# Performance work log

Measured on AMD Instinct MI355X. Metric: run time of the kernel, lower is better.

## Reference

```python
import jax, jax.numpy as jnp
import numpy as np

N = 2048       # x_dim (input features)
M = 2048       # y_dim (output features)
R0 = 1024      # components in table 0 (knn table)
D_K = 1024     # key encoder embed dim
D_V = 1024     # val encoder embed dim
BATCH = 512
ISTA_ALPHA = 1.0
ISTA_MAXITER = 5


def _ortho_encoder(key, n, d):
    # get_embedding_matrix with ortho=True: QR of (s,s) gaussian, take [:n,:d]
    s = max(n, d)
    q = jnp.linalg.qr(jax.random.normal(key, (s, s), dtype=jnp.float32))[0]
    return q[:n, :d]


def setup_inputs() -> dict:
    key = jax.random.key(0)
    kw, kk, kv, kx = jax.random.split(key, 4)
    W = jax.random.normal(kw, (N, M), dtype=jnp.float32) / np.float32(np.sqrt(N))
    # torch: V, S, U = svd(W); U = U.T  -> V = left vecs (n,k), U = right vecs (m,k)
    Usvd, S, Vh = jnp.linalg.svd(W, full_matrices=False)
    V = Usvd          # (n, k)
    Ur = Vh.T         # (m, k)
    key_enc = _ortho_encoder(kk, N, D_K)   # (n, d_k)
    val_enc = _ortho_encoder(kv, M, D_V)   # (m, d_v)
    # table 0: knn table over components [0:R0]
    keys_t0 = V[:, :R0].T @ key_enc        # (R0, d_k)
    vals_t0 = Ur[:, :R0].T @ val_enc       # (R0, d_v)
    scales_t0 = S[:R0][:, None]            # (R0, 1)
    # table 1: plain low-rank table over components [R0:]
    keys_t1 = V[:, R0:]                    # (n, R1)
    vals_t1 = Ur[:, R0:]                   # (m, R1)
    scales_t1 = S[R0:][:, None]            # (R1, 1)
    x = jax.random.normal(kx, (BATCH, N), dtype=jnp.float32)
    return {"x": x, "key_enc": key_enc, "val_enc": val_enc,
            "keys_t0": keys_t0, "vals_t0": vals_t0, "scales_t0": scales_t0,
            "keys_t1": keys_t1, "vals_t1": vals_t1, "scales_t1": scales_t1}


def _soft(x, t):
    return jnp.sign(x) * jnp.maximum(jnp.abs(x) - t, 0.0)


def reference(x, key_enc, val_enc, keys_t0, vals_t0, scales_t0,
              keys_t1, vals_t1, scales_t1):
    # --- table 0: knn path (batched; original looped over batch samples) ---
    q = x @ key_enc                        # (B, d_k)
    alphas = q @ keys_t0.T                 # (B, R0)
    betas = alphas * scales_t0.T           # (B, R0)
    yb = betas @ vals_t0                   # (B, d_v)
    # ISTA: min ||yb - z @ val_enc||^2 + alpha*||z||_1, step=1 (val_enc has
    # orthonormal columns so Lipschitz const of grad is 1)
    z = yb @ val_enc.T                     # z0, (B, m)
    for _ in range(ISTA_MAXITER):
        z = _soft(z + (yb - z @ val_enc) @ val_enc.T, ISTA_ALPHA)
    y = z                                  # knn path assigns y[b,:] = yh
    # --- table 1: low-rank path (accumulates) ---
    alphas2 = x @ keys_t1                  # (B, R1)
    betas2 = alphas2 * scales_t1.T         # (B, R1)
    y = y + betas2 @ vals_t1.T             # (B, m)
    return y
```

## Files before the change

### kernel.cpp

```cpp
#include <hip/hip_runtime.h>


typedef _Float16 f16x8 __attribute__((ext_vector_type(8)));
typedef _Float16 f16x4 __attribute__((ext_vector_type(4)));
typedef float f32x4 __attribute__((ext_vector_type(4)));

enum { EPI_H, EPI_QOFF, EPI_SPLIT, EPI_SOFT, EPI_YP, EPI_ZQ, EPI_ZQFO };

typedef const __attribute__((address_space(1))) void* gas_ptr;
typedef __attribute__((address_space(3))) void* las_ptr;

__device__ __forceinline__ void gload16(const void* g, void* l) {
  __builtin_amdgcn_global_load_lds((gas_ptr)g, (las_ptr)l, 16, 0, 0);
}

__device__ __forceinline__ float softt(float t) {
  float s = fabsf(t) - 1.0f;
  s = s > 0.0f ? s : 0.0f;
  return copysignf(s, t);
}

__global__ __launch_bounds__(256) void convAll(
    const float* __restrict__ e0, const float* __restrict__ e1,
    const float* __restrict__ e2, const float* __restrict__ e3,
    _Float16* __restrict__ o0, _Float16* __restrict__ o1,
    _Float16* __restrict__ o2, _Float16* __restrict__ o3,
    const float* __restrict__ s1, const float* __restrict__ s2,
    const float4* __restrict__ pa, f16x4* __restrict__ qa, int na,
    const float4* __restrict__ pb, f16x4* __restrict__ qb, int nb,
    const float4* __restrict__ pc, f16x4* __restrict__ qc, int nc) {
  const int z = blockIdx.z;
  if (z == 4) {
    const int total = na + nb + nc;
    const int bid = blockIdx.y * 32 + blockIdx.x;
    const int nthr = 2048 * 256;
    for (int i = bid * 256 + threadIdx.y * 32 + threadIdx.x; i < total;
         i += nthr) {
      const float4* s;
      f16x4* d;
      int j = i;
      if (j < na) {
        s = pa; d = qa;
      } else if ((j -= na) < nb) {
        s = pb; d = qb;
      } else {
        j -= nb; s = pc; d = qc;
      }
      float4 v = s[j];
      f16x4 h = {(_Float16)v.x, (_Float16)v.y, (_Float16)v.z, (_Float16)v.w};
      d[j] = h;
    }
    return;
  }
  const float* in = z == 0 ? e0 : z == 1 ? e1 : z == 2 ? e2 : e3;
  _Float16* out = z == 0 ? o0 : z == 1 ? o1 : z == 2 ? o2 : o3;
  const int R = (z < 2) ? 2048 : 1024;
  const int C = 1024;
  const int mode = z == 1 ? 1 : z == 2 ? 2 : 0;
  const float* sv = z == 1 ? s1 : s2;
  __shared__ float t[32][33];
  const int tx = threadIdx.x, ty = threadIdx.y;
  const int c0 = blockIdx.x * 32, r0 = blockIdx.y * 32;
  if (r0 >= R) return;
#pragma unroll
  for (int i = 0; i < 32; i += 8)
    t[ty + i][tx] = in[(size_t)(r0 + ty + i) * C + c0 + tx];
  __syncthreads();
#pragma unroll
  for (int i = 0; i < 32; i += 8) {
    float v = t[tx][ty + i];
    if (mode == 1) v *= sv[c0 + ty + i];
    if (mode == 2) v *= sv[r0 + tx];
    out[(size_t)(c0 + ty + i) * R + r0 + tx] = (_Float16)v;
  }
}

template <int EPI>
__device__ __forceinline__ void gtile(
    const _Float16* __restrict__ A, int lda, const _Float16* __restrict__ B,
    int ldb, int nK, int N, int brow, int bcol, float* __restrict__ dgout,
    _Float16* __restrict__ oh, _Float16* __restrict__ oh2, _Float16* sm,
    int tid) {
  const int lane = tid & 63;
  const int w = tid >> 6;
  const int wr = w & 1;
  const int wk = w >> 1;
  const int srow = lane >> 3;
  const int scol = ((lane & 7) ^ srow) << 3;
  const int a15 = lane & 15;
  const int hi = lane >> 4;
  const int l7 = lane & 7;

  const _Float16* apg = A + (size_t)(brow + (w << 4) + srow) * lda + scol;
  const _Float16* bpg = B + (size_t)(bcol + (w << 4) + srow) * ldb + scol;
  _Float16* AB = sm;
  _Float16* BB = sm + 16384;
  const int ldstA = w << 10;

  const int ca = ((wk << 2) + hi) ^ l7;
  int raddr[2], baddr[4];
#pragma unroll
  for (int mi = 0; mi < 2; ++mi)
    raddr[mi] = ((wr << 5) + (mi << 4) + a15) * 64 + (ca << 3);
#pragma unroll
  for (int ni = 0; ni < 4; ++ni)
    baddr[ni] = ((ni << 4) + a15) * 64 + (ca << 3);

  f32x4 acc[2][4] = {};

  __syncthreads();

#pragma unroll
  for (int p = 0; p < 2; ++p) {
    gload16(apg + p * 64, AB + p * 4096 + ldstA);
    gload16(apg + p * 64 + (size_t)8 * lda, AB + p * 4096 + ldstA + 512);
    gload16(bpg + p * 64, BB + p * 4096 + ldstA);
    gload16(bpg + p * 64 + (size_t)8 * ldb, BB + p * 4096 + ldstA + 512);
  }

  for (int kt = 0; kt < nK; ++kt) {
    if (kt + 2 < nK) {
      const int bf = (kt + 2) & 3;
      const int co = (kt + 2) << 6;
      gload16(apg + co, AB + bf * 4096 + ldstA);
      gload16(apg + co + (size_t)8 * lda, AB + bf * 4096 + ldstA + 512);
      gload16(bpg + co, BB + bf * 4096 + ldstA);
      gload16(bpg + co + (size_t)8 * ldb, BB + bf * 4096 + ldstA + 512);
    }
    const int rem = nK - 1 - kt;
    if (rem >= 2)
      asm volatile("s_waitcnt vmcnt(8)" ::: "memory");
    else if (rem == 1)
      asm volatile("s_waitcnt vmcnt(4)" ::: "memory");
    else
      asm volatile("s_waitcnt vmcnt(0)" ::: "memory");
    __builtin_amdgcn_s_barrier();
    __builtin_amdgcn_sched_barrier(0);
    const _Float16* Ab = AB + (kt & 3) * 4096;
    const _Float16* Bb = BB + (kt & 3) * 4096;
    f16x8 av[2], bv[4];
    av[0] = *(const f16x8*)(Ab + raddr[0]);
    av[1] = *(const f16x8*)(Ab + raddr[1]);
    bv[0] = *(const f16x8*)(Bb + baddr[0]);
    bv[1] = *(const f16x8*)(Bb + baddr[1]);
    bv[2] = *(const f16x8*)(Bb + baddr[2]);
    bv[3] = *(const f16x8*)(Bb + baddr[3]);
#pragma unroll
    for (int mi = 0; mi < 2; ++mi)
#pragma unroll
      for (int ni = 0; ni < 4; ++ni)
        acc[mi][ni] = __builtin_amdgcn_mfma_f32_16x16x32_f16(
            av[mi], bv[ni], acc[mi][ni], 0, 0, 0);
  }

  __syncthreads();
  float* scr = (float*)sm;
  const int sl = (wr << 6) + lane;
  if (wk == 1) {
#pragma unroll
    for (int mi = 0; mi < 2; ++mi)
#pragma unroll
      for (int ni = 0; ni < 4; ++ni)
#pragma unroll
        for (int r = 0; r < 4; ++r)
          scr[(((mi << 2) + ni) * 4 + r) * 128 + sl] = acc[mi][ni][r];
  }
  __syncthreads();
  if (wk == 0) {
#pragma unroll
    for (int mi = 0; mi < 2; ++mi) {
#pragma unroll
      for (int ni = 0; ni < 4; ++ni) {
#pragma unroll
        for (int r = 0; r < 4; ++r) {
          const float v =
              acc[mi][ni][r] + scr[(((mi << 2) + ni) * 4 + r) * 128 + sl];
          const int row = brow + (wr << 5) + (mi << 4) + (hi << 2) + r;
          const int col = bcol + (ni << 4) + a15;
          const size_t idx = (size_t)row * N + col;
          if constexpr (EPI == EPI_H) {
            oh[idx] = (_Float16)v;
          } else if constexpr (EPI == EPI_QOFF) {
            if (row == col) {
              dgout[row] = 1.0f - v;
              oh[idx] = (_Float16)0.0f;
            } else {
              oh[idx] = (_Float16)(-v);
            }
          } else {
            if (col < 1024)
              oh[(size_t)row * 1024 + col] = (_Float16)v;
            else
              oh2[(size_t)row * 1024 + (col - 1024)] = (_Float16)v;
          }
        }
      }
    }
  }
}

template <int EPI>
__device__ __forceinline__ void gt32(
    const _Float16* __restrict__ A, int lda, const _Float16* __restrict__ B,
    int ldb, int nK, int N, int brow, int bcol, const float* __restrict__ dgv,
    float* __restrict__ fA, float* __restrict__ fB,
    _Float16* __restrict__ oh, const float* __restrict__ fC,
    float* __restrict__ ofin, _Float16* sm, int tid) {
  const int lane = tid & 63;
  const int w = tid >> 6;
  const int wc = w & 1;
  const int wk = w >> 1;
  const int srow = lane >> 3;
  const int scol = ((lane & 7) ^ srow) << 3;
  const int a15 = lane & 15, hi = lane >> 4, l7 = lane & 7;

  const _Float16* apg = A + (size_t)(brow + (w << 3) + srow) * lda + scol;
  const _Float16* bpg = B + (size_t)(bcol + (w << 4) + srow) * ldb + scol;
  _Float16* AB = sm;
  _Float16* BB = sm + 8192;
  const int ca = ((wk << 2) + hi) ^ l7;
  int raddr[2], baddr[2];
#pragma unroll
  for (int mi = 0; mi < 2; ++mi)
    raddr[mi] = ((mi << 4) + a15) * 64 + (ca << 3);
#pragma unroll
  for (int ni = 0; ni < 2; ++ni)
    baddr[ni] = ((wc << 5) + (ni << 4) + a15) * 64 + (ca << 3);

  f32x4 acc[2][2] = {};
  __syncthreads();

#pragma unroll
  for (int p = 0; p < 2; ++p) {
    gload16(apg + p * 64, AB + p * 2048 + (w << 9));
    gload16(bpg + p * 64, BB + p * 4096 + (w << 10));
    gload16(bpg + p * 64 + (size_t)8 * ldb, BB + p * 4096 + (w << 10) + 512);
  }
  for (int kt = 0; kt < nK; ++kt) {
    if (kt + 2 < nK) {
      const int bf = (kt + 2) & 3;
      const int co = (kt + 2) << 6;
      gload16(apg + co, AB + bf * 2048 + (w << 9));
      gload16(bpg + co, BB + bf * 4096 + (w << 10));
      gload16(bpg + co + (size_t)8 * ldb, BB + bf * 4096 + (w << 10) + 512);
    }
    const int rem = nK - 1 - kt;
    if (rem >= 2)
      asm volatile("s_waitcnt vmcnt(6)" ::: "memory");
    else if (rem == 1)
      asm volatile("s_waitcnt vmcnt(3)" ::: "memory");
    else
      asm volatile("s_waitcnt vmcnt(0)" ::: "memory");
    __builtin_amdgcn_s_barrier();
    __builtin_amdgcn_sched_barrier(0);
    const _Float16* Ab = AB + (kt & 3) * 2048;
    const _Float16* Bb = BB + (kt & 3) * 4096;
    f16x8 av[2], bv[2];
    av[0] = *(const f16x8*)(Ab + raddr[0]);
    av[1] = *(const f16x8*)(Ab + raddr[1]);
    bv[0] = *(const f16x8*)(Bb + baddr[0]);
    bv[1] = *(const f16x8*)(Bb + baddr[1]);
#pragma unroll
    for (int mi = 0; mi < 2; ++mi)
#pragma unroll
      for (int ni = 0; ni < 2; ++ni)
        acc[mi][ni] = __builtin_amdgcn_mfma_f32_16x16x32_f16(
            av[mi], bv[ni], acc[mi][ni], 0, 0, 0);
  }
  __syncthreads();
  float* scr = (float*)sm;
  const int sl = (wc << 6) + lane;
  if (wk == 1) {
#pragma unroll
    for (int mi = 0; mi < 2; ++mi)
#pragma unroll
      for (int ni = 0; ni < 2; ++ni)
#pragma unroll
        for (int r = 0; r < 4; ++r)
          scr[(((mi << 1) + ni) * 4 + r) * 128 + sl] = acc[mi][ni][r];
  }
  __syncthreads();
  if (wk == 0) {
#pragma unroll
    for (int mi = 0; mi < 2; ++mi) {
#pragma unroll
      for (int ni = 0; ni < 2; ++ni) {
#pragma unroll
        for (int r = 0; r < 4; ++r) {
          const float v =
              acc[mi][ni][r] + scr[(((mi << 1) + ni) * 4 + r) * 128 + sl];
          const int row = brow + (mi << 4) + (hi << 2) + r;
          const int col = bcol + (wc << 5) + (ni << 4) + a15;
          const size_t idx = (size_t)row * N + col;
          if constexpr (EPI == EPI_SOFT) {
            fA[idx] = v;
            float s = softt(v);
            fB[idx] = s;
            oh[idx] = (_Float16)s;
          } else if constexpr (EPI == EPI_YP) {
            ofin[idx] = v;
          } else if constexpr (EPI == EPI_ZQ) {
            float t = fA[idx] + dgv[col] * fB[idx] + v;
            float s = softt(t);
            fB[idx] = s;
            oh[idx] = (_Float16)s;
          } else {
            float t = fA[idx] + dgv[col] * fB[idx] + v;
            ofin[idx] = fC[idx] + softt(t);
          }
        }
      }
    }
  }
}

struct WS {
  const _Float16 *ve, *vt1, *w0pT_r, *Bcat, *qoff_r, *x, *kt0s, *vt0T, *w0_r,
      *q_r, *be2;
  _Float16 *w0pT_w, *qoff_w, *w0_w, *q_w, *be2_w, *zhA, *zhB;
  float *z0, *zf, *dg, *yp;
};

__device__ __forceinline__ void map512(int b, int& br, int& bc) {
  const int x = b & 7, i = b >> 3;
  bc = (x << 2) | (i & 3);
  br = i >> 2;
}

__global__ __launch_bounds__(256, 2) void kD2(WS p) {
  __shared__ __align__(16) _Float16 sm[32768];
  const int tid = threadIdx.x;
  const int bid = blockIdx.x;
  if (bid < 1024) {
    gtile<EPI_QOFF>(p.ve, 1024, p.ve, 1024, 16, 2048, (bid >> 5) << 6,
                    (bid & 31) << 6, p.dg, p.qoff_w, nullptr, sm, tid);
  } else if (bid < 1280) {
    const int i = bid - 1024;
    gtile<EPI_SPLIT>(p.x, 2048, p.Bcat, 2048, 32, 2048, (i >> 5) << 6,
                     (i & 31) << 6, nullptr, p.q_w, p.be2_w, sm, tid);
  } else {
    const int i = bid - 1280;
    gtile<EPI_H>(p.kt0s, 1024, p.vt0T, 1024, 16, 1024, (i >> 4) << 6,
                 (i & 15) << 6, nullptr, p.w0_w, nullptr, sm, tid);
  }
}

__global__ __launch_bounds__(256, 2) void kW0p(WS p) {
  __shared__ __align__(16) _Float16 sm[32768];
  const int x = blockIdx.x & 7, i = blockIdx.x >> 3;
  const int bc = (x << 1) | (i & 1), br = i >> 1;
  gtile<EPI_H>(p.ve, 1024, p.w0_r, 1024, 16, 1024, br << 6, bc << 6, nullptr,
               p.w0pT_w, nullptr, sm, threadIdx.x);
}

__global__ __launch_bounds__(256, 3) void kD4(WS p) {
  __shared__ __align__(16) _Float16 sm[24576];
  const int bid = blockIdx.x;
  int br, bc;
  if (bid < 512) {
    map512(bid, br, bc);
    gt32<EPI_SOFT>(p.q_r, 1024, p.w0pT_r, 1024, 16, 2048, br << 5, bc << 6,
                   nullptr, p.z0, p.zf, p.zhA, nullptr, nullptr, sm,
                   threadIdx.x);
  } else {
    map512(bid - 512, br, bc);
    gt32<EPI_YP>(p.be2, 1024, p.vt1, 1024, 16, 2048, br << 5, bc << 6,
                 nullptr, nullptr, nullptr, nullptr, nullptr, p.yp, sm,
                 threadIdx.x);
  }
}

template <bool AB>
__global__ __launch_bounds__(256, 2) void kZQ(WS p) {
  __shared__ __align__(16) _Float16 sm[24576];
  int br, bc;
  map512(blockIdx.x, br, bc);
  gt32<EPI_ZQ>(AB ? p.zhA : p.zhB, 2048, p.qoff_r, 2048, 32, 2048, br << 5,
               bc << 6, p.dg, p.z0, p.zf, AB ? p.zhB : p.zhA, nullptr,
               nullptr, sm, threadIdx.x);
}

__global__ __launch_bounds__(256, 2) void kZQF(WS p, float* out) {
  __shared__ __align__(16) _Float16 sm[24576];
  int br, bc;
  map512(blockIdx.x, br, bc);
  gt32<EPI_ZQFO>(p.zhB, 2048, p.qoff_r, 2048, 32, 2048, br << 5, bc << 6,
                 p.dg, p.z0, p.zf, nullptr, p.yp, out, sm, threadIdx.x);
}

extern "C" void kernel_launch(void* const* d_in, const int* in_sizes, int n_in,
                              void* d_out, int out_size, void* d_ws,
                              size_t ws_size, hipStream_t stream) {
  const float* x = (const float*)d_in[0];
  const float* key_enc = (const float*)d_in[1];
  const float* val_enc = (const float*)d_in[2];
  const float* keys_t0 = (const float*)d_in[3];
  const float* vals_t0 = (const float*)d_in[4];
  const float* scales_t0 = (const float*)d_in[5];
  const float* keys_t1 = (const float*)d_in[6];
  const float* vals_t1 = (const float*)d_in[7];
  const float* scales_t1 = (const float*)d_in[8];

  constexpr size_t M1 = 1048576;
  _Float16* ws = (_Float16*)d_ws;
  _Float16* ve_h = ws;
  float* yp = (float*)ws;
  _Float16* vt1_h = ws + 2 * M1;
  _Float16* w0pT = ws + 4 * M1;
  _Float16* Bcat = ws + 6 * M1;
  _Float16* zhA = ws + 6 * M1;
  float* z0_f = (float*)(ws + 7 * M1);
  _Float16* zhB = ws + 9 * M1;
  _Float16* qoff = ws + 10 * M1;
  _Float16* x_h = ws + 14 * M1;
  _Float16* kt0s = ws + 15 * M1;
  float* z_f = (float*)(ws + 15 * M1);
  _Float16* vt0T = ws + 16 * M1;
  _Float16* w0 = ws + 17 * M1;
  _Float16* q_h = ws + 18 * M1;
  _Float16* be2 = ws + 18 * M1 + 524288;
  float* dg = (float*)(ws + 19 * M1);

  WS p;
  p.ve = ve_h; p.vt1 = vt1_h; p.w0pT_r = w0pT; p.w0pT_w = w0pT;
  p.Bcat = Bcat; p.qoff_r = qoff; p.qoff_w = qoff; p.x = x_h;
  p.kt0s = kt0s; p.vt0T = vt0T; p.w0_r = w0; p.w0_w = w0;
  p.q_r = q_h; p.q_w = q_h; p.be2 = be2; p.be2_w = be2;
  p.zhA = zhA; p.zhB = zhB; p.z0 = z0_f; p.zf = z_f; p.dg = dg; p.yp = yp;

  convAll<<<dim3(32, 64, 5), dim3(32, 8), 0, stream>>>(
      key_enc, keys_t1, keys_t0, vals_t0, Bcat, Bcat + 2 * M1, kt0s, vt0T,
      scales_t1, scales_t0, (const float4*)x, (f16x4*)x_h, 262144,
      (const float4*)val_enc, (f16x4*)ve_h, 524288, (const float4*)vals_t1,
      (f16x4*)vt1_h, 524288);
  kD2<<<1536, 256, 0, stream>>>(p);
  kW0p<<<512, 256, 0, stream>>>(p);
  kD4<<<1024, 256, 0, stream>>>(p);
  kZQ<true><<<512, 256, 0, stream>>>(p);
  kZQ<false><<<512, 256, 0, stream>>>(p);
  kZQ<true><<<512, 256, 0, stream>>>(p);
  kZQF<<<512, 256, 0, stream>>>(p, (float*)d_out);
}
```

Baseline: 110.3 us.

## Rebalance QOFF Gram tiles across kD2/kD3/kD4 to even out launch loads

The 1024 QOFF tiles (val_enc Gram-based operator) move out of kD2. Half of them join the w0p GEMM in a new kD3 kernel, and the other half join kD4 next to the soft-threshold and low-rank GEMMs. This spreads work more evenly across the dependent launches and fills idle CUs in the smaller kernels. yp is moved to its own workspace region so it no longer aliases ve_h, which QOFF tiles in kD4 still read. kD4 now uses the larger shared buffer with occupancy 2, down from 3, which may lower occupancy for the gt32 tiles.

```diff
diff --git a/kernel.cpp b/kernel.cpp
--- a/kernel.cpp
+++ b/kernel.cpp
@@ -331,42 +331,50 @@
   __shared__ __align__(16) _Float16 sm[32768];
   const int tid = threadIdx.x;
   const int bid = blockIdx.x;
-  if (bid < 1024) {
-    gtile<EPI_QOFF>(p.ve, 1024, p.ve, 1024, 16, 2048, (bid >> 5) << 6,
-                    (bid & 31) << 6, p.dg, p.qoff_w, nullptr, sm, tid);
-  } else if (bid < 1280) {
-    const int i = bid - 1024;
-    gtile<EPI_SPLIT>(p.x, 2048, p.Bcat, 2048, 32, 2048, (i >> 5) << 6,
-                     (i & 31) << 6, nullptr, p.q_w, p.be2_w, sm, tid);
+  if (bid < 256) {
+    gtile<EPI_SPLIT>(p.x, 2048, p.Bcat, 2048, 32, 2048, (bid >> 5) << 6,
+                     (bid & 31) << 6, nullptr, p.q_w, p.be2_w, sm, tid);
   } else {
-    const int i = bid - 1280;
+    const int i = bid - 256;
     gtile<EPI_H>(p.kt0s, 1024, p.vt0T, 1024, 16, 1024, (i >> 4) << 6,
                  (i & 15) << 6, nullptr, p.w0_w, nullptr, sm, tid);
   }
 }
 
-__global__ __launch_bounds__(256, 2) void kW0p(WS p) {
+__global__ __launch_bounds__(256, 2) void kD3(WS p) {
   __shared__ __align__(16) _Float16 sm[32768];
-  const int x = blockIdx.x & 7, i = blockIdx.x >> 3;
-  const int bc = (x << 1) | (i & 1), br = i >> 1;
-  gtile<EPI_H>(p.ve, 1024, p.w0_r, 1024, 16, 1024, br << 6, bc << 6, nullptr,
-               p.w0pT_w, nullptr, sm, threadIdx.x);
-}
-
-__global__ __launch_bounds__(256, 3) void kD4(WS p) {
-  __shared__ __align__(16) _Float16 sm[24576];
+  const int tid = threadIdx.x;
+  const int bid = blockIdx.x;
+  if (bid < 512) {
+    const int x = bid & 7, i = bid >> 3;
+    const int bc = (x << 1) | (i & 1), br = i >> 1;
+    gtile<EPI_H>(p.ve, 1024, p.w0_r, 1024, 16, 1024, br << 6, bc << 6,
+                 nullptr, p.w0pT_w, nullptr, sm, tid);
+  } else {
+    const int i = bid - 512;
+    gtile<EPI_QOFF>(p.ve, 1024, p.ve, 1024, 16, 2048, (i >> 5) << 6,
+                    (i & 31) << 6, p.dg, p.qoff_w, nullptr, sm, tid);
+  }
+}
+
+__global__ __launch_bounds__(256, 2) void kD4(WS p) {
+  __shared__ __align__(16) _Float16 sm[32768];
+  const int tid = threadIdx.x;
   const int bid = blockIdx.x;
   int br, bc;
   if (bid < 512) {
     map512(bid, br, bc);
     gt32<EPI_SOFT>(p.q_r, 1024, p.w0pT_r, 1024, 16, 2048, br << 5, bc << 6,
-                   nullptr, p.z0, p.zf, p.zhA, nullptr, nullptr, sm,
-                   threadIdx.x);
+                   nullptr, p.z0, p.zf, p.zhA, nullptr, nullptr, sm, tid);
+  } else if (bid < 1024) {
+    const int i = bid - 512;
+    gtile<EPI_QOFF>(p.ve, 1024, p.ve, 1024, 16, 2048,
+                    (16 + (i >> 5)) << 6, (i & 31) << 6, p.dg, p.qoff_w,
+                    nullptr, sm, tid);
   } else {
-    map512(bid - 512, br, bc);
+    map512(bid - 1024, br, bc);
     gt32<EPI_YP>(p.be2, 1024, p.vt1, 1024, 16, 2048, br << 5, bc << 6,
-                 nullptr, nullptr, nullptr, nullptr, nullptr, p.yp, sm,
-                 threadIdx.x);
+                 nullptr, nullptr, nullptr, nullptr, nullptr, p.yp, sm, tid);
   }
 }
 
@@ -404,7 +412,6 @@
   constexpr size_t M1 = 1048576;
   _Float16* ws = (_Float16*)d_ws;
   _Float16* ve_h = ws;
-  float* yp = (float*)ws;
   _Float16* vt1_h = ws + 2 * M1;
   _Float16* w0pT = ws + 4 * M1;
   _Float16* Bcat = ws + 6 * M1;
@@ -420,6 +427,7 @@
   _Float16* q_h = ws + 18 * M1;
   _Float16* be2 = ws + 18 * M1 + 524288;
   float* dg = (float*)(ws + 19 * M1);
+  float* yp = (float*)(ws + 20 * M1);
 
   WS p;
   p.ve = ve_h; p.vt1 = vt1_h; p.w0pT_r = w0pT; p.w0pT_w = w0pT;
@@ -433,9 +441,9 @@
       scales_t1, scales_t0, (const float4*)x, (f16x4*)x_h, 262144,
       (const float4*)val_enc, (f16x4*)ve_h, 524288, (const float4*)vals_t1,
       (f16x4*)vt1_h, 524288);
-  kD2<<<1536, 256, 0, stream>>>(p);
-  kW0p<<<512, 256, 0, stream>>>(p);
-  kD4<<<1024, 256, 0, stream>>>(p);
+  kD2<<<512, 256, 0, stream>>>(p);
+  kD3<<<1024, 256, 0, stream>>>(p);
+  kD4<<<1536, 256, 0, stream>>>(p);
   kZQ<true><<<512, 256, 0, stream>>>(p);
   kZQ<false><<<512, 256, 0, stream>>>(p);
   kZQ<true><<<512, 256, 0, stream>>>(p);
```

Result: no change. 111.2 us (+0.9%).

## Switch GEMM tiles to 32x32x16 MFMA with four-way split-K reduction

Applied to the files above, without the earlier changes.

Both GEMM tile routines replace 16x16x32 MFMA with 32x32x16 MFMA. Each of the four waves now handles a distinct 16-element K slice of the 64-wide K tile, instead of two waves splitting M/N and two splitting K. The epilogue becomes a four-way reduction through shared memory, with two waves each finalizing half the outputs. This aims for larger MFMA shapes and fewer LDS fragment reads, at the cost of a heavier cross-wave reduction and more accumulator registers. It also lowers kD4 launch bounds from 3 to 2 blocks per CU.

```diff
diff --git a/kernel.cpp b/kernel.cpp
--- a/kernel.cpp
+++ b/kernel.cpp
@@ -4,6 +4,7 @@
 typedef _Float16 f16x8 __attribute__((ext_vector_type(8)));
 typedef _Float16 f16x4 __attribute__((ext_vector_type(4)));
 typedef float f32x4 __attribute__((ext_vector_type(4)));
+typedef float f32x16 __attribute__((ext_vector_type(16)));
 
 enum { EPI_H, EPI_QOFF, EPI_SPLIT, EPI_SOFT, EPI_YP, EPI_ZQ, EPI_ZQFO };
 
@@ -76,56 +77,55 @@
 }
 
 template <int EPI>
-__device__ __forceinline__ void gtile(
+__device__ __forceinline__ void g64(
     const _Float16* __restrict__ A, int lda, const _Float16* __restrict__ B,
     int ldb, int nK, int N, int brow, int bcol, float* __restrict__ dgout,
     _Float16* __restrict__ oh, _Float16* __restrict__ oh2, _Float16* sm,
     int tid) {
   const int lane = tid & 63;
   const int w = tid >> 6;
-  const int wr = w & 1;
-  const int wk = w >> 1;
   const int srow = lane >> 3;
   const int scol = ((lane & 7) ^ srow) << 3;
-  const int a15 = lane & 15;
-  const int hi = lane >> 4;
+  const int r31 = lane & 31;
+  const int hi5 = lane >> 5;
   const int l7 = lane & 7;
 
   const _Float16* apg = A + (size_t)(brow + (w << 4) + srow) * lda + scol;
   const _Float16* bpg = B + (size_t)(bcol + (w << 4) + srow) * ldb + scol;
   _Float16* AB = sm;
   _Float16* BB = sm + 16384;
-  const int ldstA = w << 10;
-
-  const int ca = ((wk << 2) + hi) ^ l7;
-  int raddr[2], baddr[4];
+  const int ldst = w << 10;
+
+  const int swz = ((w << 1) + hi5) ^ l7;
+  int raddr[2], baddr[2];
 #pragma unroll
   for (int mi = 0; mi < 2; ++mi)
-    raddr[mi] = ((wr << 5) + (mi << 4) + a15) * 64 + (ca << 3);
-#pragma unroll
-  for (int ni = 0; ni < 4; ++ni)
-    baddr[ni] = ((ni << 4) + a15) * 64 + (ca << 3);
-
-  f32x4 acc[2][4] = {};
+    raddr[mi] = ((mi << 5) + r31) * 64 + (swz << 3);
+#pragma unroll
+  for (int ni = 0; ni < 2; ++ni)
+    baddr[ni] = ((ni << 5) + r31) * 64 + (swz << 3);
+
+  f32x16 acc[2][2] = {};
 
   __syncthreads();
 
 #pragma unroll
   for (int p = 0; p < 2; ++p) {
-    gload16(apg + p * 64, AB + p * 4096 + ldstA);
-    gload16(apg + p * 64 + (size_t)8 * lda, AB + p * 4096 + ldstA + 512);
-    gload16(bpg + p * 64, BB + p * 4096 + ldstA);
-    gload16(bpg + p * 64 + (size_t)8 * ldb, BB + p * 4096 + ldstA + 512);
+    const int co = p << 6;
+    gload16(apg + co, AB + p * 4096 + ldst);
+    gload16(apg + co + (size_t)8 * lda, AB + p * 4096 + ldst + 512);
+    gload16(bpg + co, BB + p * 4096 + ldst);
+    gload16(bpg + co + (size_t)8 * ldb, BB + p * 4096 + ldst + 512);
   }
 
   for (int kt = 0; kt < nK; ++kt) {
     if (kt + 2 < nK) {
       const int bf = (kt + 2) & 3;
       const int co = (kt + 2) << 6;
-      gload16(apg + co, AB + bf * 4096 + ldstA);
-      gload16(apg + co + (size_t)8 * lda, AB + bf * 4096 + ldstA + 512);
-      gload16(bpg + co, BB + bf * 4096 + ldstA);
-      gload16(bpg + co + (size_t)8 * ldb, BB + bf * 4096 + ldstA + 512);
+      gload16(apg + co, AB + bf * 4096 + ldst);
+      gload16(apg + co + (size_t)8 * lda, AB + bf * 4096 + ldst + 512);
+      gload16(bpg + co, BB + bf * 4096 + ldst);
+      gload16(bpg + co + (size_t)8 * ldb, BB + bf * 4096 + ldst + 512);
     }
     const int rem = nK - 1 - kt;
     if (rem >= 2)
@@ -138,69 +138,88 @@
     __builtin_amdgcn_sched_barrier(0);
     const _Float16* Ab = AB + (kt & 3) * 4096;
     const _Float16* Bb = BB + (kt & 3) * 4096;
-    f16x8 av[2], bv[4];
+    f16x8 av[2], bv[2];
     av[0] = *(const f16x8*)(Ab + raddr[0]);
     av[1] = *(const f16x8*)(Ab + raddr[1]);
     bv[0] = *(const f16x8*)(Bb + baddr[0]);
     bv[1] = *(const f16x8*)(Bb + baddr[1]);
-    bv[2] = *(const f16x8*)(Bb + baddr[2]);
-    bv[3] = *(const f16x8*)(Bb + baddr[3]);
 #pragma unroll
     for (int mi = 0; mi < 2; ++mi)
 #pragma unroll
-      for (int ni = 0; ni < 4; ++ni)
-        acc[mi][ni] = __builtin_amdgcn_mfma_f32_16x16x32_f16(
+      for (int ni = 0; ni < 2; ++ni)
+        acc[mi][ni] = __builtin_amdgcn_mfma_f32_32x32x16_f16(
             av[mi], bv[ni], acc[mi][ni], 0, 0, 0);
   }
 
   __syncthreads();
   float* scr = (float*)sm;
-  const int sl = (wr << 6) + lane;
-  if (wk == 1) {
+  if (w >= 2) {
 #pragma unroll
     for (int mi = 0; mi < 2; ++mi)
 #pragma unroll
-      for (int ni = 0; ni < 4; ++ni)
-#pragma unroll
-        for (int r = 0; r < 4; ++r)
-          scr[(((mi << 2) + ni) * 4 + r) * 128 + sl] = acc[mi][ni][r];
-  }
-  __syncthreads();
-  if (wk == 0) {
-#pragma unroll
-    for (int mi = 0; mi < 2; ++mi) {
-#pragma unroll
-      for (int ni = 0; ni < 4; ++ni) {
-#pragma unroll
-        for (int r = 0; r < 4; ++r) {
-          const float v =
-              acc[mi][ni][r] + scr[(((mi << 2) + ni) * 4 + r) * 128 + sl];
-          const int row = brow + (wr << 5) + (mi << 4) + (hi << 2) + r;
-          const int col = bcol + (ni << 4) + a15;
-          const size_t idx = (size_t)row * N + col;
-          if constexpr (EPI == EPI_H) {
-            oh[idx] = (_Float16)v;
-          } else if constexpr (EPI == EPI_QOFF) {
-            if (row == col) {
-              dgout[row] = 1.0f - v;
-              oh[idx] = (_Float16)0.0f;
-            } else {
-              oh[idx] = (_Float16)(-v);
-            }
-          } else {
-            if (col < 1024)
-              oh[(size_t)row * 1024 + col] = (_Float16)v;
-            else
-              oh2[(size_t)row * 1024 + (col - 1024)] = (_Float16)v;
-          }
+      for (int ni = 0; ni < 2; ++ni)
+#pragma unroll
+        for (int r = 0; r < 16; ++r)
+          scr[((((mi << 1) + ni) * 3 + (w - 1)) * 16 + r) * 64 + lane] =
+              acc[mi][ni][r];
+  } else if (w == 0) {
+#pragma unroll
+    for (int ni = 0; ni < 2; ++ni)
+#pragma unroll
+      for (int r = 0; r < 16; ++r)
+        scr[(((2 + ni) * 3 + 0) * 16 + r) * 64 + lane] = acc[1][ni][r];
+  } else {
+#pragma unroll
+    for (int ni = 0; ni < 2; ++ni)
+#pragma unroll
+      for (int r = 0; r < 16; ++r)
+        scr[((ni * 3 + 0) * 16 + r) * 64 + lane] = acc[0][ni][r];
+  }
+  __syncthreads();
+  if (w >= 2) return;
+  f32x16 own[2];
+  if (w == 0) {
+    own[0] = acc[0][0];
+    own[1] = acc[0][1];
+  } else {
+    own[0] = acc[1][0];
+    own[1] = acc[1][1];
+  }
+#pragma unroll
+  for (int ni = 0; ni < 2; ++ni) {
+#pragma unroll
+    for (int j = 0; j < 3; ++j)
+#pragma unroll
+      for (int r = 0; r < 16; ++r)
+        own[ni][r] += scr[((((w << 1) + ni) * 3 + j) * 16 + r) * 64 + lane];
+#pragma unroll
+    for (int r = 0; r < 16; ++r) {
+      const int row =
+          brow + (w << 5) + (r & 3) + (((r >> 2)) << 3) + (hi5 << 2);
+      const int col = bcol + (ni << 5) + r31;
+      const float v = own[ni][r];
+      const size_t idx = (size_t)row * N + col;
+      if constexpr (EPI == EPI_H) {
+        oh[idx] = (_Float16)v;
+      } else if constexpr (EPI == EPI_QOFF) {
+        if (row == col) {
+          dgout[row] = 1.0f - v;
+          oh[idx] = (_Float16)0.0f;
+        } else {
+          oh[idx] = (_Float16)(-v);
         }
+      } else {
+        if (col < 1024)
+          oh[(size_t)row * 1024 + col] = (_Float16)v;
+        else
+          oh2[(size_t)row * 1024 + (col - 1024)] = (_Float16)v;
       }
     }
   }
 }
 
 template <int EPI>
-__device__ __forceinline__ void gt32(
+__device__ __forceinline__ void g32n(
     const _Float16* __restrict__ A, int lda, const _Float16* __restrict__ B,
     int ldb, int nK, int N, int brow, int bcol, const float* __restrict__ dgv,
     float* __restrict__ fA, float* __restrict__ fB,
@@ -208,33 +227,32 @@
     float* __restrict__ ofin, _Float16* sm, int tid) {
   const int lane = tid & 63;
   const int w = tid >> 6;
-  const int wc = w & 1;
-  const int wk = w >> 1;
   const int srow = lane >> 3;
   const int scol = ((lane & 7) ^ srow) << 3;
-  const int a15 = lane & 15, hi = lane >> 4, l7 = lane & 7;
+  const int r31 = lane & 31;
+  const int hi5 = lane >> 5;
+  const int l7 = lane & 7;
 
   const _Float16* apg = A + (size_t)(brow + (w << 3) + srow) * lda + scol;
   const _Float16* bpg = B + (size_t)(bcol + (w << 4) + srow) * ldb + scol;
   _Float16* AB = sm;
   _Float16* BB = sm + 8192;
-  const int ca = ((wk << 2) + hi) ^ l7;
-  int raddr[2], baddr[2];
-#pragma unroll
-  for (int mi = 0; mi < 2; ++mi)
-    raddr[mi] = ((mi << 4) + a15) * 64 + (ca << 3);
+  const int swz = ((w << 1) + hi5) ^ l7;
+  const int raddr0 = r31 * 64 + (swz << 3);
+  int baddr[2];
 #pragma unroll
   for (int ni = 0; ni < 2; ++ni)
-    baddr[ni] = ((wc << 5) + (ni << 4) + a15) * 64 + (ca << 3);
-
-  f32x4 acc[2][2] = {};
+    baddr[ni] = ((ni << 5) + r31) * 64 + (swz << 3);
+
+  f32x16 acc[2] = {};
   __syncthreads();
 
 #pragma unroll
   for (int p = 0; p < 2; ++p) {
-    gload16(apg + p * 64, AB + p * 2048 + (w << 9));
-    gload16(bpg + p * 64, BB + p * 4096 + (w << 10));
-    gload16(bpg + p * 64 + (size_t)8 * ldb, BB + p * 4096 + (w << 10) + 512);
+    const int co = p << 6;
+    gload16(apg + co, AB + p * 2048 + (w << 9));
+    gload16(bpg + co, BB + p * 4096 + (w << 10));
+    gload16(bpg + co + (size_t)8 * ldb, BB + p * 4096 + (w << 10) + 512);
   }
   for (int kt = 0; kt < nK; ++kt) {
     if (kt + 2 < nK) {
@@ -255,61 +273,61 @@
     __builtin_amdgcn_sched_barrier(0);
     const _Float16* Ab = AB + (kt & 3) * 2048;
     const _Float16* Bb = BB + (kt & 3) * 4096;
-    f16x8 av[2], bv[2];
-    av[0] = *(const f16x8*)(Ab + raddr[0]);
-    av[1] = *(const f16x8*)(Ab + raddr[1]);
-    bv[0] = *(const f16x8*)(Bb + baddr[0]);
-    bv[1] = *(const f16x8*)(Bb + baddr[1]);
-#pragma unroll
-    for (int mi = 0; mi < 2; ++mi)
-#pragma unroll
-      for (int ni = 0; ni < 2; ++ni)
-        acc[mi][ni] = __builtin_amdgcn_mfma_f32_16x16x32_f16(
-            av[mi], bv[ni], acc[mi][ni], 0, 0, 0);
-  }
+    f16x8 av = *(const f16x8*)(Ab + raddr0);
+    f16x8 bv0 = *(const f16x8*)(Bb + baddr[0]);
+    f16x8 bv1 = *(const f16x8*)(Bb + baddr[1]);
+    acc[0] =
+        __builtin_amdgcn_mfma_f32_32x32x16_f16(av, bv0, acc[0], 0, 0, 0);
+    acc[1] =
+        __builtin_amdgcn_mfma_f32_32x32x16_f16(av, bv1, acc[1], 0, 0, 0);
+  }
+
   __syncthreads();
   float* scr = (float*)sm;
-  const int sl = (wc << 6) + lane;
-  if (wk == 1) {
-#pragma unroll
-    for (int mi = 0; mi < 2; ++mi)
-#pragma unroll
-      for (int ni = 0; ni < 2; ++ni)
-#pragma unroll
-        for (int r = 0; r < 4; ++r)
-          scr[(((mi << 1) + ni) * 4 + r) * 128 + sl] = acc[mi][ni][r];
-  }
-  __syncthreads();
-  if (wk == 0) {
-#pragma unroll
-    for (int mi = 0; mi < 2; ++mi) {
-#pragma unroll
-      for (int ni = 0; ni < 2; ++ni) {
-#pragma unroll
-        for (int r = 0; r < 4; ++r) {
-          const float v =
-              acc[mi][ni][r] + scr[(((mi << 1) + ni) * 4 + r) * 128 + sl];
-          const int row = brow + (mi << 4) + (hi << 2) + r;
-          const int col = bcol + (wc << 5) + (ni << 4) + a15;
-          const size_t idx = (size_t)row * N + col;
-          if constexpr (EPI == EPI_SOFT) {
-            fA[idx] = v;
-            float s = softt(v);
-            fB[idx] = s;
-            oh[idx] = (_Float16)s;
-          } else if constexpr (EPI == EPI_YP) {
-            ofin[idx] = v;
-          } else if constexpr (EPI == EPI_ZQ) {
-            float t = fA[idx] + dgv[col] * fB[idx] + v;
-            float s = softt(t);
-            fB[idx] = s;
-            oh[idx] = (_Float16)s;
-          } else {
-            float t = fA[idx] + dgv[col] * fB[idx] + v;
-            ofin[idx] = fC[idx] + softt(t);
-          }
-        }
-      }
+  if (w >= 2) {
+#pragma unroll
+    for (int ni = 0; ni < 2; ++ni)
+#pragma unroll
+      for (int r = 0; r < 16; ++r)
+        scr[((ni * 3 + (w - 1)) * 16 + r) * 64 + lane] = acc[ni][r];
+  } else if (w == 0) {
+#pragma unroll
+    for (int r = 0; r < 16; ++r)
+      scr[((1 * 3 + 0) * 16 + r) * 64 + lane] = acc[1][r];
+  } else {
+#pragma unroll
+    for (int r = 0; r < 16; ++r)
+      scr[((0 * 3 + 0) * 16 + r) * 64 + lane] = acc[0][r];
+  }
+  __syncthreads();
+  if (w >= 2) return;
+  f32x16 own = (w == 0) ? acc[0] : acc[1];
+#pragma unroll
+  for (int j = 0; j < 3; ++j)
+#pragma unroll
+    for (int r = 0; r < 16; ++r)
+      own[r] += scr[((w * 3 + j) * 16 + r) * 64 + lane];
+#pragma unroll
+  for (int r = 0; r < 16; ++r) {
+    const int row = brow + (r & 3) + ((r >> 2) << 3) + (hi5 << 2);
+    const int col = bcol + (w << 5) + r31;
+    const float v = own[r];
+    const size_t idx = (size_t)row * N + col;
+    if constexpr (EPI == EPI_SOFT) {
+      fA[idx] = v;
+      float s = softt(v);
+      fB[idx] = s;
+      oh[idx] = (_Float16)s;
+    } else if constexpr (EPI == EPI_YP) {
+      ofin[idx] = v;
+    } else if constexpr (EPI == EPI_ZQ) {
+      float t = fA[idx] + dgv[col] * fB[idx] + v;
+      float s = softt(t);
+      fB[idx] = s;
+      oh[idx] = (_Float16)s;
+    } else {
+      float t = fA[idx] + dgv[col] * fB[idx] + v;
+      ofin[idx] = fC[idx] + softt(t);
     }
   }
 }
@@ -332,16 +350,16 @@
   const int tid = threadIdx.x;
   const int bid = blockIdx.x;
   if (bid < 1024) {
-    gtile<EPI_QOFF>(p.ve, 1024, p.ve, 1024, 16, 2048, (bid >> 5) << 6,
-                    (bid & 31) << 6, p.dg, p.qoff_w, nullptr, sm, tid);
+    g64<EPI_QOFF>(p.ve, 1024, p.ve, 1024, 16, 2048, (bid >> 5) << 6,
+                  (bid & 31) << 6, p.dg, p.qoff_w, nullptr, sm, tid);
   } else if (bid < 1280) {
     const int i = bid - 1024;
-    gtile<EPI_SPLIT>(p.x, 2048, p.Bcat, 2048, 32, 2048, (i >> 5) << 6,
-                     (i & 31) << 6, nullptr, p.q_w, p.be2_w, sm, tid);
+    g64<EPI_SPLIT>(p.x, 2048, p.Bcat, 2048, 32, 2048, (i >> 5) << 6,
+                   (i & 31) << 6, nullptr, p.q_w, p.be2_w, sm, tid);
   } else {
     const int i = bid - 1280;
-    gtile<EPI_H>(p.kt0s, 1024, p.vt0T, 1024, 16, 1024, (i >> 4) << 6,
-                 (i & 15) << 6, nullptr, p.w0_w, nullptr, sm, tid);
+    g64<EPI_H>(p.kt0s, 1024, p.vt0T, 1024, 16, 1024, (i >> 4) << 6,
+               (i & 15) << 6, nullptr, p.w0_w, nullptr, sm, tid);
   }
 }
 
@@ -349,22 +367,22 @@
   __shared__ __align__(16) _Float16 sm[32768];
   const int x = blockIdx.x & 7, i = blockIdx.x >> 3;
   const int bc = (x << 1) | (i & 1), br = i >> 1;
-  gtile<EPI_H>(p.ve, 1024, p.w0_r, 1024, 16, 1024, br << 6, bc << 6, nullptr,
-               p.w0pT_w, nullptr, sm, threadIdx.x);
-}
-
-__global__ __launch_bounds__(256, 3) void kD4(WS p) {
+  g64<EPI_H>(p.ve, 1024, p.w0_r, 1024, 16, 1024, br << 6, bc << 6, nullptr,
+             p.w0pT_w, nullptr, sm, threadIdx.x);
+}
+
+__global__ __launch_bounds__(256, 2) void kD4(WS p) {
   __shared__ __align__(16) _Float16 sm[24576];
   const int bid = blockIdx.x;
   int br, bc;
   if (bid < 512) {
     map512(bid, br, bc);
-    gt32<EPI_SOFT>(p.q_r, 1024, p.w0pT_r, 1024, 16, 2048, br << 5, bc << 6,
+    g32n<EPI_SOFT>(p.q_r, 1024, p.w0pT_r, 1024, 16, 2048, br << 5, bc << 6,
                    nullptr, p.z0, p.zf, p.zhA, nullptr, nullptr, sm,
                    threadIdx.x);
   } else {
     map512(bid - 512, br, bc);
-    gt32<EPI_YP>(p.be2, 1024, p.vt1, 1024, 16, 2048, br << 5, bc << 6,
+    g32n<EPI_YP>(p.be2, 1024, p.vt1, 1024, 16, 2048, br << 5, bc << 6,
                  nullptr, nullptr, nullptr, nullptr, nullptr, p.yp, sm,
                  threadIdx.x);
   }
@@ -375,7 +393,7 @@
   __shared__ __align__(16) _Float16 sm[24576];
   int br, bc;
   map512(blockIdx.x, br, bc);
-  gt32<EPI_ZQ>(AB ? p.zhA : p.zhB, 2048, p.qoff_r, 2048, 32, 2048, br << 5,
+  g32n<EPI_ZQ>(AB ? p.zhA : p.zhB, 2048, p.qoff_r, 2048, 32, 2048, br << 5,
                bc << 6, p.dg, p.z0, p.zf, AB ? p.zhB : p.zhA, nullptr,
                nullptr, sm, threadIdx.x);
 }
@@ -384,7 +402,7 @@
   __shared__ __align__(16) _Float16 sm[24576];
   int br, bc;
   map512(blockIdx.x, br, bc);
-  gt32<EPI_ZQFO>(p.zhB, 2048, p.qoff_r, 2048, 32, 2048, br << 5, bc << 6,
+  g32n<EPI_ZQFO>(p.zhB, 2048, p.qoff_r, 2048, 32, 2048, br << 5, bc << 6,
                  p.dg, p.z0, p.zf, nullptr, p.yp, out, sm, threadIdx.x);
 }
 
```

New measurement: 112.0 us. No clear change (+1.6%).
